# Optimization experiments

Hardware: AMD Instinct MI355X
Metric: run time of the kernel (lower is better)

The kernel has to match this reference:

```python
import jax, jax.numpy as jnp
import numpy as np

HIDDEN_DIM = 2048
HEAD_NUM = 16
HEAD_DIM = HIDDEN_DIM // HEAD_NUM


def setup_inputs() -> dict:
    key = jax.random.key(0)
    ks = jax.random.split(key, 9)
    B, S, H = 2, 2048, HIDDEN_DIM
    scale = 1.0 / np.sqrt(H)
    X = jax.random.normal(ks[0], (B, S, H), dtype=jnp.float32)
    Wq = jax.random.normal(ks[1], (H, H), dtype=jnp.float32) * scale
    bq = jnp.zeros((H,), dtype=jnp.float32)
    Wk = jax.random.normal(ks[2], (H, H), dtype=jnp.float32) * scale
    bk = jnp.zeros((H,), dtype=jnp.float32)
    Wv = jax.random.normal(ks[3], (H, H), dtype=jnp.float32) * scale
    bv = jnp.zeros((H,), dtype=jnp.float32)
    Wo = jax.random.normal(ks[4], (H, H), dtype=jnp.float32) * scale
    bo = jnp.zeros((H,), dtype=jnp.float32)
    return {"X": X, "Wq": Wq, "bq": bq, "Wk": Wk, "bk": bk,
            "Wv": Wv, "bv": bv, "Wo": Wo, "bo": bo}


def reference(X, Wq, bq, Wk, bk, Wv, bv, Wo, bo):
    B, S, H = X.shape
    # QKV projections (nn.Linear applies x @ W.T + b; weights here stored as [in, out])
    Q = X @ Wq + bq
    K = X @ Wk + bk
    V = X @ Wv + bv
    # [B, heads, S, head_dim]
    q = Q.reshape(B, S, HEAD_NUM, HEAD_DIM).transpose(0, 2, 1, 3)
    k = K.reshape(B, S, HEAD_NUM, HEAD_DIM).transpose(0, 2, 1, 3)
    v = V.reshape(B, S, HEAD_NUM, HEAD_DIM).transpose(0, 2, 1, 3)
    scores = jnp.einsum('bhqd,bhkd->bhqk', q, k) / jnp.sqrt(jnp.float32(HEAD_DIM))
    attn = jax.nn.softmax(scores, axis=-1)  # dropout = identity in eval
    out = jnp.einsum('bhqk,bhkd->bhqd', attn, v)
    out = out.transpose(0, 2, 1, 3).reshape(B, S, H)
    return out @ Wo + bo
```

## Files before the change

kernel.cpp:

```cpp
#include <hip/hip_runtime.h>
#include <hip/hip_bf16.h>
#include <stdint.h>


#define Bc 2
#define Sc 2048
#define Hc 2048
#define NHc 16
#define Dc 128
#define Mc 4096

typedef unsigned short ushortT;
typedef float f32x4 __attribute__((ext_vector_type(4)));
typedef _Float16 f16x8 __attribute__((ext_vector_type(8)));

#define MFMAH(a, b, c) __builtin_amdgcn_mfma_f32_16x16x32_f16((a), (b), (c), 0, 0, 0)

static __device__ __forceinline__ ushortT f2h(float x) {
    _Float16 h = (_Float16)x;
    return __builtin_bit_cast(unsigned short, h);
}

static __device__ __forceinline__ void load_lds16(const ushortT* g, ushortT* l) {
    __builtin_amdgcn_global_load_lds(
        (__attribute__((address_space(1))) void*)(g),
        (__attribute__((address_space(3))) void*)(l), 16, 0, 0);
}

__global__ __launch_bounds__(256) void pack_a(
    const float* __restrict__ src, ushortT* __restrict__ dst)
{
    const int mt = blockIdx.x, kt = blockIdx.y;
    const int t = threadIdx.x;
    const int kq = t & 15;
    const int r0 = t >> 4;
    ushortT* tile = dst + ((size_t)(mt * 32 + kt)) * 8192;
#pragma unroll
    for (int rr = 0; rr < 8; ++rr) {
        const int row = r0 + rr * 16;
        const float4 v = *(const float4*)(src + (size_t)(mt * 128 + row) * Hc + kt * 64 + kq * 4);
        _Float16 h[4] = {(_Float16)v.x, (_Float16)v.y, (_Float16)v.z, (_Float16)v.w};
        const int gid = kq >> 1, halfg = kq & 1;
        const int gp = gid ^ (row & 7);
        *(uint2*)(tile + (size_t)row * 64 + gp * 8 + halfg * 4) = *(uint2*)h;
    }
}

__global__ __launch_bounds__(256) void pack_b(
    const float* __restrict__ W0, const float* __restrict__ W1,
    const float* __restrict__ W2, const float* __restrict__ W3,
    ushortT* __restrict__ dst)
{
    const int nt = blockIdx.x, kt = blockIdx.y, which = blockIdx.z;
    const float* W = (which == 0) ? W0 : (which == 1) ? W1 : (which == 2) ? W2 : W3;
    const int t = threadIdx.x;
    const int n = t & 127;
    const int g0 = (t >> 7) * 4;
    ushortT* tile = dst + (size_t)which * 4194304 + ((size_t)(nt * 32 + kt)) * 8192;
#pragma unroll
    for (int gi = 0; gi < 4; ++gi) {
        const int g = g0 + gi;
        _Float16 h[8];
#pragma unroll
        for (int j = 0; j < 8; ++j)
            h[j] = (_Float16)W[(size_t)(kt * 64 + g * 8 + j) * Hc + nt * 128 + n];
        const int gp = g ^ (n & 7);
        *(uint4*)(tile + (size_t)n * 64 + gp * 8) = *(uint4*)h;
    }
}

#define GEMM_PROLOGUE()                                                        \
    __shared__ __align__(16) ushortT As[8192], Bs[8192];                       \
    const int tid = threadIdx.x, wv_ = tid >> 6, lane = tid & 63;              \
    const int lane16 = lane & 15, quad = lane >> 4;                            \
    const int quad4 = quad * 4;                                                \
    const int wm = (wv_ & 1) * 64, wn = (wv_ >> 1) * 64;                       \
    int aoff[4][2], boff[4][2];                                                \
    _Pragma("unroll") for (int mi = 0; mi < 4; ++mi)                           \
        _Pragma("unroll") for (int kf = 0; kf < 2; ++kf) {                     \
            const int ra = wm + mi * 16 + lane16;                              \
            aoff[mi][kf] = ra * 64 + (((kf * 4 + quad) ^ (ra & 7)) << 3);      \
            const int rb = wn + mi * 16 + lane16;                              \
            boff[mi][kf] = rb * 64 + (((kf * 4 + quad) ^ (rb & 7)) << 3);      \
        }                                                                      \
    f32x4 acc[4][4];                                                           \
    _Pragma("unroll") for (int i = 0; i < 4; ++i)                              \
        _Pragma("unroll") for (int j = 0; j < 4; ++j) {                        \
            acc[i][j][0] = 0.f; acc[i][j][1] = 0.f;                            \
            acc[i][j][2] = 0.f; acc[i][j][3] = 0.f; }                          \
    ushortT* asd = &As[wv_ * 2048];                                            \
    ushortT* bsd = &Bs[wv_ * 2048];

#define GEMM_KLOOP(at, bt)                                                     \
    for (int kt2 = 0; kt2 < 32; ++kt2) {                                       \
        _Pragma("unroll") for (int i = 0; i < 4; ++i) {                        \
            load_lds16(at + i * 512 + lane * 8, asd + i * 512);                \
            load_lds16(bt + i * 512 + lane * 8, bsd + i * 512);                \
        }                                                                      \
        at += 8192; bt += 8192;                                                \
        __syncthreads();                                                       \
        _Pragma("unroll") for (int kf = 0; kf < 2; ++kf) {                     \
            f16x8 a[4], b[4];                                                  \
            _Pragma("unroll") for (int mi = 0; mi < 4; ++mi)                   \
                a[mi] = *(const f16x8*)&As[aoff[mi][kf]];                      \
            _Pragma("unroll") for (int nj = 0; nj < 4; ++nj)                   \
                b[nj] = *(const f16x8*)&Bs[boff[nj][kf]];                      \
            _Pragma("unroll") for (int nj = 0; nj < 4; ++nj)                   \
                _Pragma("unroll") for (int mi = 0; mi < 4; ++mi)               \
                    acc[mi][nj] = MFMAH(a[mi], b[nj], acc[mi][nj]);            \
        }                                                                      \
        __syncthreads();                                                       \
    }

__global__ __launch_bounds__(256) void qkv_gemm(
    const ushortT* __restrict__ Xp, const ushortT* __restrict__ Wall,
    const float* __restrict__ bq, const float* __restrict__ bk,
    const float* __restrict__ bv,
    ushortT* __restrict__ Qd, ushortT* __restrict__ Kd, ushortT* __restrict__ Vt)
{
    const int which = blockIdx.x >> 4;
    const int nt = blockIdx.x & 15;
    const int mt = blockIdx.y;
    const ushortT* Wp = Wall + (size_t)which * 4194304;
    const float* bias = (which == 0) ? bq : (which == 1) ? bk : bv;

    GEMM_PROLOGUE();

    const ushortT* at = Xp + (size_t)(mt * 32) * 8192 + wv_ * 2048;
    const ushortT* bt = Wp + (size_t)(nt * 32) * 8192 + wv_ * 2048;
    GEMM_KLOOP(at, bt);

    const float QS = 0.08838834764831845f * 1.4426950408889634f;
#pragma unroll
    for (int nj = 0; nj < 4; ++nj) {
        const int col = nt * 128 + wn + nj * 16 + lane16;
        const float bb = bias[col];
        const int hh = col >> 7, dd = col & 127;
#pragma unroll
        for (int mi = 0; mi < 4; ++mi)
#pragma unroll
            for (int r = 0; r < 4; ++r) {
                const int m = mt * 128 + wm + mi * 16 + quad4 + r;
                const int b = m >> 11, s = m & 2047;
                const float v = acc[mi][nj][r] + bb;
                const size_t bhb = (size_t)(b * NHc + hh) * (Sc * Dc);
                if (which == 0) {
                    Qd[bhb + (size_t)s * Dc + dd] = f2h(v * QS);
                } else if (which == 1) {
                    const int t2 = s >> 6, sin = s & 63;
                    Kd[bhb + (size_t)t2 * 8192 + sin * 128 +
                       (((dd >> 3) ^ (sin & 7)) << 3) + (dd & 7)] = f2h(v);
                } else {
                    const int t2 = s >> 6, sin = s & 63;
                    Vt[bhb + (size_t)t2 * 8192 + dd * 64 +
                       (((sin >> 3) ^ (dd & 7)) << 3) + (sin & 7)] = f2h(v);
                }
            }
    }
}

__global__ __launch_bounds__(128, 2) void attn(
    const ushortT* __restrict__ Qd, const ushortT* __restrict__ Kt,
    const ushortT* __restrict__ Vt, ushortT* __restrict__ AOp)
{
    const int id = blockIdx.x;
    const int slot = id >> 3;
    const int pair = (id & 7) + ((slot >> 5) << 3);
    const int qt = slot & 31;
    const int hh = pair & 15, bb = pair >> 4;

    const ushortT* Qp  = Qd + ((size_t)(bb * NHc + hh)) * Sc * Dc;
    const ushortT* Kbh = Kt + ((size_t)(bb * NHc + hh)) * Sc * Dc;
    const ushortT* Vbh = Vt + ((size_t)(bb * NHc + hh)) * Sc * Dc;

    __shared__ __align__(16) ushortT Ks[8192];
    __shared__ __align__(16) ushortT Vs[8192];
    __shared__ __align__(16) ushortT Pbuf[2][2048];

    const int tid = threadIdx.x, wv_ = tid >> 6, lane = tid & 63;
    const int lane16 = lane & 15, quad = lane >> 4;
    const int quad8 = quad * 8, quad4 = quad * 4;
    const int s0 = qt * 64 + wv_ * 32;

    f16x8 q[2][4];
#pragma unroll
    for (int nj = 0; nj < 2; ++nj)
#pragma unroll
        for (int kf = 0; kf < 4; ++kf)
            q[nj][kf] = *(const f16x8*)(Qp + (size_t)(s0 + nj * 16 + lane16) * Dc + kf * 32 + quad8);

    f32x4 o[8][2];
#pragma unroll
    for (int dj = 0; dj < 8; ++dj)
#pragma unroll
        for (int nj = 0; nj < 2; ++nj) { o[dj][nj][0] = 0.f; o[dj][nj][1] = 0.f; o[dj][nj][2] = 0.f; o[dj][nj][3] = 0.f; }

    float m_run[2] = {-1e30f, -1e30f}, l_run[2] = {0.f, 0.f};
    ushortT* Pw = Pbuf[wv_];

    for (int nt = 0; nt < 32; ++nt) {
        const ushortT* ktile = Kbh + (size_t)nt * 8192 + wv_ * 4096;
        const ushortT* vtile = Vbh + (size_t)nt * 8192 + wv_ * 4096;
#pragma unroll
        for (int i = 0; i < 8; ++i) {
            load_lds16(ktile + i * 512 + lane * 8, Ks + wv_ * 4096 + i * 512);
            load_lds16(vtile + i * 512 + lane * 8, Vs + wv_ * 4096 + i * 512);
        }
        __syncthreads();

        f32x4 sacc[4][2];
#pragma unroll
        for (int mi = 0; mi < 4; ++mi)
#pragma unroll
            for (int nj = 0; nj < 2; ++nj) { sacc[mi][nj][0] = 0.f; sacc[mi][nj][1] = 0.f; sacc[mi][nj][2] = 0.f; sacc[mi][nj][3] = 0.f; }
#pragma unroll
        for (int kf = 0; kf < 4; ++kf) {
            f16x8 kb[4];
#pragma unroll
            for (int mi = 0; mi < 4; ++mi) {
                const int row = mi * 16 + lane16;
                kb[mi] = *(const f16x8*)&Ks[row * 128 + (((kf * 4 + quad) ^ (row & 7)) << 3)];
            }
#pragma unroll
            for (int mi = 0; mi < 4; ++mi)
#pragma unroll
                for (int nj = 0; nj < 2; ++nj)
                    sacc[mi][nj] = MFMAH(kb[mi], q[nj][kf], sacc[mi][nj]);
        }

        float alpha_[2];
#pragma unroll
        for (int nj = 0; nj < 2; ++nj) {
            float mx = sacc[0][nj][0];
#pragma unroll
            for (int mi = 0; mi < 4; ++mi)
#pragma unroll
                for (int r = 0; r < 4; ++r) mx = fmaxf(mx, sacc[mi][nj][r]);
            mx = fmaxf(mx, __shfl_xor(mx, 16));
            mx = fmaxf(mx, __shfl_xor(mx, 32));
            const float mnew = fmaxf(m_run[nj], mx);
            alpha_[nj] = exp2f(m_run[nj] - mnew);
            m_run[nj] = mnew;
            float sum = 0.f;
#pragma unroll
            for (int mi = 0; mi < 4; ++mi)
#pragma unroll
                for (int r = 0; r < 4; ++r) {
                    const float p = exp2f(sacc[mi][nj][r] - mnew);
                    sacc[mi][nj][r] = p;
                    sum += p;
                }
            sum += __shfl_xor(sum, 16);
            sum += __shfl_xor(sum, 32);
            l_run[nj] = l_run[nj] * alpha_[nj] + sum;
            const int prow = nj * 16 + lane16;
#pragma unroll
            for (int mi = 0; mi < 4; ++mi) {
                uint2 u;
                u.x = (uint32_t)f2h(sacc[mi][nj][0]) | ((uint32_t)f2h(sacc[mi][nj][1]) << 16);
                u.y = (uint32_t)f2h(sacc[mi][nj][2]) | ((uint32_t)f2h(sacc[mi][nj][3]) << 16);
                const int g = mi * 2 + (quad >> 1);
                *(uint2*)&Pw[prow * 64 + ((g ^ (prow & 7)) << 3) + (quad & 1) * 4] = u;
            }
        }

#pragma unroll
        for (int dj = 0; dj < 8; ++dj)
#pragma unroll
            for (int nj = 0; nj < 2; ++nj) {
                const float av = alpha_[nj];
                o[dj][nj][0] *= av; o[dj][nj][1] *= av;
                o[dj][nj][2] *= av; o[dj][nj][3] *= av;
            }

#pragma unroll
        for (int kf2 = 0; kf2 < 2; ++kf2) {
            f16x8 pb[2];
#pragma unroll
            for (int nj = 0; nj < 2; ++nj) {
                const int row = nj * 16 + lane16;
                pb[nj] = *(const f16x8*)&Pw[row * 64 + (((kf2 * 4 + quad) ^ (row & 7)) << 3)];
            }
#pragma unroll
            for (int dj = 0; dj < 8; ++dj) {
                const int row = dj * 16 + lane16;
                const f16x8 vb = *(const f16x8*)&Vs[row * 64 + (((kf2 * 4 + quad) ^ (row & 7)) << 3)];
#pragma unroll
                for (int nj = 0; nj < 2; ++nj)
                    o[dj][nj] = MFMAH(vb, pb[nj], o[dj][nj]);
            }
        }
        __syncthreads();
    }

#pragma unroll
    for (int nj = 0; nj < 2; ++nj) {
        const float inv = 1.f / l_run[nj];
        const int m = bb * Sc + qt * 64 + wv_ * 32 + nj * 16 + lane16;
        const int mtile = m >> 7, rin = m & 127;
#pragma unroll
        for (int dj = 0; dj < 8; ++dj) {
            const int ktile = hh * 2 + (dj >> 2);
            const int cin0 = (dj & 3) * 16 + quad4;
            const int g = cin0 >> 3, e0 = cin0 & 7;
            uint2 u;
            u.x = (uint32_t)f2h(o[dj][nj][0] * inv) | ((uint32_t)f2h(o[dj][nj][1] * inv) << 16);
            u.y = (uint32_t)f2h(o[dj][nj][2] * inv) | ((uint32_t)f2h(o[dj][nj][3] * inv) << 16);
            *(uint2*)&AOp[((size_t)(mtile * 32 + ktile)) * 8192 + rin * 64 +
                          ((g ^ (rin & 7)) << 3) + e0] = u;
        }
    }
}

__global__ __launch_bounds__(256) void out_gemm(
    const ushortT* __restrict__ AOp, const ushortT* __restrict__ Wop,
    const float* __restrict__ bo, float* __restrict__ out)
{
    const int nt = blockIdx.x;
    const int mt = blockIdx.y;

    GEMM_PROLOGUE();

    const ushortT* at = AOp + (size_t)(mt * 32) * 8192 + wv_ * 2048;
    const ushortT* bt = Wop + (size_t)(nt * 32) * 8192 + wv_ * 2048;
    GEMM_KLOOP(at, bt);

#pragma unroll
    for (int nj = 0; nj < 4; ++nj) {
        const int col = nt * 128 + wn + nj * 16 + lane16;
        const float bb = bo[col];
#pragma unroll
        for (int mi = 0; mi < 4; ++mi)
#pragma unroll
            for (int r = 0; r < 4; ++r) {
                const int m = mt * 128 + wm + mi * 16 + quad4 + r;
                out[(size_t)m * Hc + col] = acc[mi][nj][r] + bb;
            }
    }
}

extern "C" void kernel_launch(void* const* d_in, const int* in_sizes, int n_in,
                              void* d_out, int out_size, void* d_ws, size_t ws_size,
                              hipStream_t stream) {
    (void)in_sizes; (void)n_in; (void)out_size; (void)ws_size;

    const float* X  = (const float*)d_in[0];
    const float* Wq = (const float*)d_in[1];
    const float* bq = (const float*)d_in[2];
    const float* Wk = (const float*)d_in[3];
    const float* bk = (const float*)d_in[4];
    const float* Wv = (const float*)d_in[5];
    const float* bv = (const float*)d_in[6];
    const float* Wo = (const float*)d_in[7];
    const float* bo = (const float*)d_in[8];
    float* out = (float*)d_out;

    ushortT* ws = (ushortT*)d_ws;
    const size_t E = (size_t)Mc * Hc;
    const size_t WE = (size_t)Hc * Hc;
    ushortT* Xp   = ws;
    ushortT* Wall = Xp + E;
    ushortT* Qd   = Wall + 4 * WE;
    ushortT* Kd   = Qd + E;
    ushortT* Vtp  = Kd + E;
    ushortT* AOp  = Vtp + E;

    pack_a<<<dim3(32, 32), 256, 0, stream>>>(X, Xp);
    pack_b<<<dim3(16, 32, 4), 256, 0, stream>>>(Wq, Wk, Wv, Wo, Wall);
    qkv_gemm<<<dim3(48, 32), 256, 0, stream>>>(Xp, Wall, bq, bk, bv, Qd, Kd, Vtp);
    attn<<<dim3(1024), 128, 0, stream>>>(Qd, Kd, Vtp, AOp);
    out_gemm<<<dim3(16, 32), 256, 0, stream>>>(AOp, Wall + 3 * WE, bo, out);
}
```

Before: 448.1 us.

## Rewrite projection GEMMs as 256x256 double-buffered pipelined kernels with block swizzle

Replaces the 128x128, 4-wave GEMM (single LDS buffer, two syncs per k-step) used by the QKV and output projections with a 256x256, 8-wave kernel. The new kernel double-buffers LDS, interleaves async global-to-LDS loads with MFMA quads, gates them with explicit vmcnt waits and barriers, and raises wave priority during MFMA sections. Block IDs are swizzled for better L2 locality. The goal is to hide load latency and double arithmetic intensity per LDS byte, at the cost of more registers and fewer blocks (128 for the output GEMM), which may underfill the 256 CUs.

Result: slower. 501.6 us (+11.9%).

```diff
diff --git a/kernel.cpp b/kernel.cpp
--- a/kernel.cpp
+++ b/kernel.cpp
@@ -69,91 +69,155 @@
     }
 }
 
-#define GEMM_PROLOGUE()                                                        \
-    __shared__ __align__(16) ushortT As[8192], Bs[8192];                       \
+#define G256_PROLOGUE()                                                        \
+    __shared__ __align__(16) ushortT LA[2][2][8192];                           \
+    __shared__ __align__(16) ushortT LB[2][2][8192];                           \
     const int tid = threadIdx.x, wv_ = tid >> 6, lane = tid & 63;              \
-    const int lane16 = lane & 15, quad = lane >> 4;                            \
-    const int quad4 = quad * 4;                                                \
-    const int wm = (wv_ & 1) * 64, wn = (wv_ >> 1) * 64;                       \
-    int aoff[4][2], boff[4][2];                                                \
-    _Pragma("unroll") for (int mi = 0; mi < 4; ++mi)                           \
-        _Pragma("unroll") for (int kf = 0; kf < 2; ++kf) {                     \
-            const int ra = wm + mi * 16 + lane16;                              \
-            aoff[mi][kf] = ra * 64 + (((kf * 4 + quad) ^ (ra & 7)) << 3);      \
-            const int rb = wn + mi * 16 + lane16;                              \
-            boff[mi][kf] = rb * 64 + (((kf * 4 + quad) ^ (rb & 7)) << 3);      \
-        }                                                                      \
-    f32x4 acc[4][4];                                                           \
-    _Pragma("unroll") for (int i = 0; i < 4; ++i)                              \
+    const int lane16 = lane & 15, quad = lane >> 4, quad4 = (lane >> 4) * 4;   \
+    const int wr = wv_ >> 2, wc = wv_ & 3;                                     \
+    f32x4 acc[8][4];                                                           \
+    _Pragma("unroll") for (int i = 0; i < 8; ++i)                              \
         _Pragma("unroll") for (int j = 0; j < 4; ++j) {                        \
             acc[i][j][0] = 0.f; acc[i][j][1] = 0.f;                            \
-            acc[i][j][2] = 0.f; acc[i][j][3] = 0.f; }                          \
-    ushortT* asd = &As[wv_ * 2048];                                            \
-    ushortT* bsd = &Bs[wv_ * 2048];
-
-#define GEMM_KLOOP(at, bt)                                                     \
-    for (int kt2 = 0; kt2 < 32; ++kt2) {                                       \
-        _Pragma("unroll") for (int i = 0; i < 4; ++i) {                        \
-            load_lds16(at + i * 512 + lane * 8, asd + i * 512);                \
-            load_lds16(bt + i * 512 + lane * 8, bsd + i * 512);                \
-        }                                                                      \
-        at += 8192; bt += 8192;                                                \
-        __syncthreads();                                                       \
-        _Pragma("unroll") for (int kf = 0; kf < 2; ++kf) {                     \
-            f16x8 a[4], b[4];                                                  \
-            _Pragma("unroll") for (int mi = 0; mi < 4; ++mi)                   \
-                a[mi] = *(const f16x8*)&As[aoff[mi][kf]];                      \
-            _Pragma("unroll") for (int nj = 0; nj < 4; ++nj)                   \
-                b[nj] = *(const f16x8*)&Bs[boff[nj][kf]];                      \
-            _Pragma("unroll") for (int nj = 0; nj < 4; ++nj)                   \
-                _Pragma("unroll") for (int mi = 0; mi < 4; ++mi)               \
-                    acc[mi][nj] = MFMAH(a[mi], b[nj], acc[mi][nj]);            \
-        }                                                                      \
-        __syncthreads();                                                       \
-    }
-
-__global__ __launch_bounds__(256) void qkv_gemm(
+            acc[i][j][2] = 0.f; acc[i][j][3] = 0.f; }
+
+#define STAGE(GT, LDST) do {                                                   \
+    const ushortT* g_ = (GT) + wv_ * 1024 + lane * 8;                          \
+    ushortT* l_ = (LDST) + wv_ * 1024;                                         \
+    load_lds16(g_, l_);                                                        \
+    load_lds16(g_ + 512, l_ + 512);                                            \
+} while (0)
+
+#define RD_A(S, RB)                                                            \
+    _Pragma("unroll") for (int mi = 0; mi < 4; ++mi) {                         \
+        const int r_ = (RB) + mi * 16 + lane16;                                \
+        _Pragma("unroll") for (int kf = 0; kf < 2; ++kf)                       \
+            a[mi][kf] = *(const f16x8*)&LA[S][wr][r_ * 64 +                    \
+                (((kf * 4 + quad) ^ (r_ & 7)) << 3)];                          \
+    }
+
+#define RD_B(S)                                                                \
+    _Pragma("unroll") for (int nj = 0; nj < 4; ++nj) {                         \
+        const int r_ = (wc & 1) * 64 + nj * 16 + lane16;                       \
+        _Pragma("unroll") for (int kf = 0; kf < 2; ++kf)                       \
+            b[nj][kf] = *(const f16x8*)&LB[S][wc >> 1][r_ * 64 +               \
+                (((kf * 4 + quad) ^ (r_ & 7)) << 3)];                          \
+    }
+
+#define QUAD(MIB, NJB)                                                         \
+    _Pragma("unroll") for (int kf = 0; kf < 2; ++kf)                           \
+        _Pragma("unroll") for (int mi = 0; mi < 4; ++mi)                       \
+            _Pragma("unroll") for (int nj = 0; nj < 2; ++nj)                   \
+                acc[(MIB) + mi][(NJB) + nj] =                                  \
+                    MFMAH(a[mi][kf], b[(NJB) + nj][kf], acc[(MIB) + mi][(NJB) + nj]);
+
+#define PRE_MFMA()                                                             \
+    __builtin_amdgcn_sched_barrier(0);                                         \
+    __builtin_amdgcn_s_barrier();                                              \
+    __builtin_amdgcn_sched_barrier(0);                                         \
+    __builtin_amdgcn_s_setprio(1);
+
+#define POST_MFMA()                                                            \
+    __builtin_amdgcn_s_setprio(0);                                             \
+    __builtin_amdgcn_sched_barrier(0);                                         \
+    __builtin_amdgcn_s_barrier();                                              \
+    __builtin_amdgcn_sched_barrier(0);
+
+#define VMC6() asm volatile("s_waitcnt vmcnt(6)" ::: "memory")
+
+#define MINS(x) ((x) < 31 ? (x) : 31)
+
+#define G256_MAIN(AB0, AB1, BB0, BB1)                                          \
+      \
+    STAGE(BB0, &LB[0][0][0]); STAGE(BB1, &LB[0][1][0]);                        \
+    STAGE(AB0, &LA[0][0][0]); STAGE(AB1, &LA[0][1][0]);                        \
+    STAGE(BB0 + 8192, &LB[1][0][0]); STAGE(BB1 + 8192, &LB[1][1][0]);          \
+    STAGE(AB0 + 8192, &LA[1][0][0]);                                           \
+    VMC6();                                                                    \
+    __builtin_amdgcn_sched_barrier(0);                                         \
+    __builtin_amdgcn_s_barrier();                                              \
+    __builtin_amdgcn_sched_barrier(0);                                         \
+    _Pragma("clang loop unroll(disable)")                                      \
+    for (int t = 0; t < 32; t += 2) {                                          \
+        f16x8 a[4][2], b[4][2];                                                \
+                                \
+        RD_A(0, 0); RD_B(0);                                                   \
+        STAGE(AB1 + (size_t)(t + 1) * 8192, &LA[1][1][0]);                     \
+        PRE_MFMA(); QUAD(0, 0); POST_MFMA();                                   \
+                                            \
+        STAGE(BB0 + (size_t)MINS(t + 2) * 8192, &LB[0][0][0]);                 \
+        PRE_MFMA(); QUAD(0, 2); POST_MFMA();                                   \
+                                                       \
+        RD_A(0, 64);                                                           \
+        STAGE(BB1 + (size_t)MINS(t + 2) * 8192, &LB[0][1][0]);                 \
+        PRE_MFMA(); QUAD(4, 2); POST_MFMA();                                   \
+            \
+        STAGE(AB0 + (size_t)MINS(t + 2) * 8192, &LA[0][0][0]);                 \
+        VMC6();                                                                \
+        PRE_MFMA(); QUAD(4, 0); POST_MFMA();                                   \
+                                             \
+        RD_A(1, 0); RD_B(1);                                                   \
+        STAGE(AB1 + (size_t)MINS(t + 2) * 8192, &LA[0][1][0]);                 \
+        PRE_MFMA(); QUAD(0, 0); POST_MFMA();                                   \
+                                                                       \
+        STAGE(BB0 + (size_t)MINS(t + 3) * 8192, &LB[1][0][0]);                 \
+        PRE_MFMA(); QUAD(0, 2); POST_MFMA();                                   \
+                                                                       \
+        RD_A(1, 64);                                                           \
+        STAGE(BB1 + (size_t)MINS(t + 3) * 8192, &LB[1][1][0]);                 \
+        PRE_MFMA(); QUAD(4, 2); POST_MFMA();                                   \
+                            \
+        STAGE(AB0 + (size_t)MINS(t + 3) * 8192, &LA[1][0][0]);                 \
+        VMC6();                                                                \
+        PRE_MFMA(); QUAD(4, 0); POST_MFMA();                                   \
+    }
+
+__global__ __launch_bounds__(512, 2) void qkv_gemm256(
     const ushortT* __restrict__ Xp, const ushortT* __restrict__ Wall,
     const float* __restrict__ bq, const float* __restrict__ bk,
     const float* __restrict__ bv,
     ushortT* __restrict__ Qd, ushortT* __restrict__ Kd, ushortT* __restrict__ Vt)
 {
-    const int which = blockIdx.x >> 4;
-    const int nt = blockIdx.x & 15;
-    const int mt = blockIdx.y;
-    const ushortT* Wp = Wall + (size_t)which * 4194304;
+    const int id = blockIdx.x;
+    const int swz = (id & 7) * 48 + (id >> 3);
+    const int mt = swz & 15;
+    const int bn = swz >> 4;
+    const int which = bn >> 3, bnw = bn & 7;
+    const ushortT* Ab0 = Xp + (size_t)((2 * mt + 0) * 32) * 8192;
+    const ushortT* Ab1 = Xp + (size_t)((2 * mt + 1) * 32) * 8192;
+    const ushortT* Wp  = Wall + (size_t)which * 4194304;
+    const ushortT* Bb0 = Wp + (size_t)((bnw * 2 + 0) * 32) * 8192;
+    const ushortT* Bb1 = Wp + (size_t)((bnw * 2 + 1) * 32) * 8192;
     const float* bias = (which == 0) ? bq : (which == 1) ? bk : bv;
 
-    GEMM_PROLOGUE();
-
-    const ushortT* at = Xp + (size_t)(mt * 32) * 8192 + wv_ * 2048;
-    const ushortT* bt = Wp + (size_t)(nt * 32) * 8192 + wv_ * 2048;
-    GEMM_KLOOP(at, bt);
+    G256_PROLOGUE();
+    G256_MAIN(Ab0, Ab1, Bb0, Bb1);
+    asm volatile("s_waitcnt vmcnt(0)" ::: "memory");
 
     const float QS = 0.08838834764831845f * 1.4426950408889634f;
 #pragma unroll
     for (int nj = 0; nj < 4; ++nj) {
-        const int col = nt * 128 + wn + nj * 16 + lane16;
-        const float bb = bias[col];
-        const int hh = col >> 7, dd = col & 127;
-#pragma unroll
-        for (int mi = 0; mi < 4; ++mi)
+        const int colm = bnw * 256 + wc * 64 + nj * 16 + lane16;
+        const float bb2 = bias[colm];
+        const int hh = colm >> 7, dd = colm & 127;
+#pragma unroll
+        for (int mi = 0; mi < 8; ++mi)
 #pragma unroll
             for (int r = 0; r < 4; ++r) {
-                const int m = mt * 128 + wm + mi * 16 + quad4 + r;
+                const int m = mt * 256 + wr * 128 + mi * 16 + quad4 + r;
                 const int b = m >> 11, s = m & 2047;
-                const float v = acc[mi][nj][r] + bb;
+                const float v = acc[mi][nj][r] + bb2;
                 const size_t bhb = (size_t)(b * NHc + hh) * (Sc * Dc);
                 if (which == 0) {
                     Qd[bhb + (size_t)s * Dc + dd] = f2h(v * QS);
                 } else if (which == 1) {
-                    const int t2 = s >> 6, sin = s & 63;
-                    Kd[bhb + (size_t)t2 * 8192 + sin * 128 +
-                       (((dd >> 3) ^ (sin & 7)) << 3) + (dd & 7)] = f2h(v);
+                    const int t2 = s >> 6, sin_ = s & 63;
+                    Kd[bhb + (size_t)t2 * 8192 + sin_ * 128 +
+                       (((dd >> 3) ^ (sin_ & 7)) << 3) + (dd & 7)] = f2h(v);
                 } else {
-                    const int t2 = s >> 6, sin = s & 63;
+                    const int t2 = s >> 6, sin_ = s & 63;
                     Vt[bhb + (size_t)t2 * 8192 + dd * 64 +
-                       (((sin >> 3) ^ (dd & 7)) << 3) + (sin & 7)] = f2h(v);
+                       (((sin_ >> 3) ^ (dd & 7)) << 3) + (sin_ & 7)] = f2h(v);
                 }
             }
     }
@@ -312,29 +376,33 @@
     }
 }
 
-__global__ __launch_bounds__(256) void out_gemm(
+__global__ __launch_bounds__(512, 2) void out_gemm256(
     const ushortT* __restrict__ AOp, const ushortT* __restrict__ Wop,
     const float* __restrict__ bo, float* __restrict__ out)
 {
-    const int nt = blockIdx.x;
-    const int mt = blockIdx.y;
-
-    GEMM_PROLOGUE();
-
-    const ushortT* at = AOp + (size_t)(mt * 32) * 8192 + wv_ * 2048;
-    const ushortT* bt = Wop + (size_t)(nt * 32) * 8192 + wv_ * 2048;
-    GEMM_KLOOP(at, bt);
+    const int id = blockIdx.x;
+    const int swz = (id & 7) * 16 + (id >> 3);
+    const int mt = swz & 15;
+    const int bn = swz >> 4;
+    const ushortT* Ab0 = AOp + (size_t)((2 * mt + 0) * 32) * 8192;
+    const ushortT* Ab1 = AOp + (size_t)((2 * mt + 1) * 32) * 8192;
+    const ushortT* Bb0 = Wop + (size_t)((bn * 2 + 0) * 32) * 8192;
+    const ushortT* Bb1 = Wop + (size_t)((bn * 2 + 1) * 32) * 8192;
+
+    G256_PROLOGUE();
+    G256_MAIN(Ab0, Ab1, Bb0, Bb1);
+    asm volatile("s_waitcnt vmcnt(0)" ::: "memory");
 
 #pragma unroll
     for (int nj = 0; nj < 4; ++nj) {
-        const int col = nt * 128 + wn + nj * 16 + lane16;
-        const float bb = bo[col];
-#pragma unroll
-        for (int mi = 0; mi < 4; ++mi)
+        const int col = bn * 256 + wc * 64 + nj * 16 + lane16;
+        const float bb2 = bo[col];
+#pragma unroll
+        for (int mi = 0; mi < 8; ++mi)
 #pragma unroll
             for (int r = 0; r < 4; ++r) {
-                const int m = mt * 128 + wm + mi * 16 + quad4 + r;
-                out[(size_t)m * Hc + col] = acc[mi][nj][r] + bb;
+                const int m = mt * 256 + wr * 128 + mi * 16 + quad4 + r;
+                out[(size_t)m * Hc + col] = acc[mi][nj][r] + bb2;
             }
     }
 }
@@ -367,7 +435,7 @@
 
     pack_a<<<dim3(32, 32), 256, 0, stream>>>(X, Xp);
     pack_b<<<dim3(16, 32, 4), 256, 0, stream>>>(Wq, Wk, Wv, Wo, Wall);
-    qkv_gemm<<<dim3(48, 32), 256, 0, stream>>>(Xp, Wall, bq, bk, bv, Qd, Kd, Vtp);
+    qkv_gemm256<<<dim3(384), 512, 0, stream>>>(Xp, Wall, bq, bk, bv, Qd, Kd, Vtp);
     attn<<<dim3(1024), 128, 0, stream>>>(Qd, Kd, Vtp, AOp);
-    out_gemm<<<dim3(16, 32), 256, 0, stream>>>(AOp, Wall + 3 * WE, bo, out);
-}
+    out_gemm256<<<dim3(128), 512, 0, stream>>>(AOp, Wall + 3 * WE, bo, out);
+}
```
